# Kernel optimization log

Measured on AMD Instinct MI355X. Metric: run time of the kernel, lower is better.

Reference implementation:

```python
import jax, jax.numpy as jnp
import numpy as np

N, E = 20000, 640000
LATENT, HID, OUT, HEADS = 512, 256, 128, 2
NEG_SLOPE = 0.2


def setup_inputs() -> dict:
    key = jax.random.key(0)
    ks = jax.random.split(key, 12)
    s = 0.02
    return {
        "z": jax.random.normal(ks[0], (N, LATENT), dtype=jnp.float32),
        "edge_index": jax.random.randint(ks[1], (2, E), 0, N, dtype=jnp.int64),
        "W1": jax.random.normal(ks[2], (LATENT, HID), dtype=jnp.float32) * s,
        "b1": jnp.zeros((HID,), dtype=jnp.float32),
        "W2": jax.random.normal(ks[3], (HID, HID * HEADS), dtype=jnp.float32) * s,
        "b2": jnp.zeros((HID * HEADS,), dtype=jnp.float32),
        "Wg": jax.random.normal(ks[4], (HID * HEADS, HEADS * OUT), dtype=jnp.float32) * s,
        "att_src": jax.random.normal(ks[5], (HEADS, OUT), dtype=jnp.float32) * s,
        "att_dst": jax.random.normal(ks[6], (HEADS, OUT), dtype=jnp.float32) * s,
        "bias_g": jnp.zeros((HEADS * OUT,), dtype=jnp.float32),
        "W3": jax.random.normal(ks[7], (OUT * HEADS, 512), dtype=jnp.float32) * s,
        "b3": jnp.zeros((512,), dtype=jnp.float32),
    }


def _gat_conv(x, edge_index, Wg, att_src, att_dst, bias_g):
    n = x.shape[0]
    # add self loops (PyG GATConv default add_self_loops=True)
    loops = jnp.tile(jnp.arange(n, dtype=edge_index.dtype)[None, :], (2, 1))
    ei = jnp.concatenate([edge_index, loops], axis=1)
    src, dst = ei[0], ei[1]
    xp = (x @ Wg).reshape(n, HEADS, OUT)          # [N,H,C]
    a_src = jnp.einsum('nhc,hc->nh', xp, att_src)  # [N,H]
    a_dst = jnp.einsum('nhc,hc->nh', xp, att_dst)
    alpha = jax.nn.leaky_relu(a_src[src] + a_dst[dst], NEG_SLOPE)  # [E+N,H]
    amax = jax.ops.segment_max(alpha, dst, num_segments=n)
    alpha = jnp.exp(alpha - amax[dst])
    denom = jax.ops.segment_sum(alpha, dst, num_segments=n)
    alpha = alpha / jnp.maximum(denom[dst], 1e-16)
    msg = xp[src] * alpha[:, :, None]              # [E+N,H,C]
    out = jax.ops.segment_sum(msg, dst, num_segments=n)  # [N,H,C]
    return out.reshape(n, HEADS * OUT) + bias_g


def reference(z, edge_index, W1, b1, W2, b2, Wg, att_src, att_dst, bias_g, W3, b3):
    x = jax.nn.relu(z @ W1 + b1)
    x = jax.nn.relu(x @ W2 + b2)
    x = _gat_conv(x, edge_index, Wg, att_src, att_dst, bias_g)
    return x @ W3 + b3
```

## Files before the change

kernel.cpp:

```cpp
#include <hip/hip_runtime.h>
#include <hip/hip_bf16.h>
#include <float.h>

#define N_NODES 20000
#define LATENT  512
#define HID     256
#define OUT_C   128
#define HEADS   2
#define HC      256
#define NEG_SLOPE 0.2f

typedef _Float16 half8 __attribute__((ext_vector_type(8)));
typedef __attribute__((ext_vector_type(4))) float f32x4;

__device__ __forceinline__ ushort f2h(float v) {
    _Float16 h = (_Float16)v;
    return *(ushort*)&h;
}
__device__ __forceinline__ float h2f(ushort u) {
    _Float16 h = *(_Float16*)&u;
    return (float)h;
}

__device__ __forceinline__ void gl_lds16(const ushort* g, ushort* l) {
    __builtin_amdgcn_global_load_lds(
        (const __attribute__((address_space(1))) unsigned int*)g,
        (__attribute__((address_space(3))) unsigned int*)l, 16, 0, 0);
}

template<int BN>
__global__ __launch_bounds__(256) void gemm_f16(
    const ushort* __restrict__ A, const ushort* __restrict__ BT,
    const float* __restrict__ bias,
    float* __restrict__ Cf, ushort* __restrict__ Ch,
    int M, int N, int K, int relu)
{
    constexpr int NI  = BN / 32;
    constexpr int BUF = 4096 + BN * 32;
    __shared__ ushort lds[2 * BUF];
    ushort* buf0 = lds;
    ushort* buf1 = lds + BUF;

    const int t = threadIdx.x;
    const int l = t & 63;
    const int w = t >> 6;
    const int wm = (w >> 1) * 64;
    const int wn = (w & 1) * (BN / 2);
    const int lm = l & 15;
    const int q  = l >> 4;
    const int q4 = q * 4;

    const int row0 = blockIdx.x * 128;
    const int col0 = blockIdx.y * BN;

    const int jr0 = w * 16 + (l >> 2);
    const int gsh = (((l & 3) ^ ((l >> 4) & 3)) << 3);
    const ushort* gA0 = A + (size_t)(row0 + jr0) * K + gsh;
    const ushort* gA1 = gA0 + (size_t)64 * K;
    const ushort* gB0 = BT + (size_t)(col0 + jr0) * K + gsh;
    const ushort* gB1 = gB0 + (size_t)64 * K;
    const int dA0 = w * 512, dA1 = (4 + w) * 512;
    const int dB0 = 4096 + w * 512, dB1 = 4096 + (4 + w) * 512;

    const int csw = ((q ^ ((lm >> 2) & 3)) << 3);

    const f32x4 zf = {0.f, 0.f, 0.f, 0.f};
    f32x4 acc[4][NI];
    #pragma unroll
    for (int i = 0; i < 4; ++i)
        #pragma unroll
        for (int j = 0; j < NI; ++j) acc[i][j] = zf;

    auto issue = [&](int kk, ushort* B) {
        gl_lds16(gA0 + kk, B + dA0);
        gl_lds16(gA1 + kk, B + dA1);
        gl_lds16(gB0 + kk, B + dB0);
        if (BN == 128) gl_lds16(gB1 + kk, B + dB1);
    };

    auto compute = [&](const ushort* B) {
        half8 bf[NI];
        #pragma unroll
        for (int ni = 0; ni < NI; ++ni) {
            const int boff = (wn + ni * 16 + lm) * 32 + csw;
            bf[ni] = *(const half8*)&B[4096 + boff];
        }
        #pragma unroll
        for (int mi = 0; mi < 4; ++mi) {
            const int aoff = (wm + mi * 16 + lm) * 32 + csw;
            half8 af = *(const half8*)&B[aoff];
            #pragma unroll
            for (int ni = 0; ni < NI; ++ni)
                acc[mi][ni] = __builtin_amdgcn_mfma_f32_16x16x32_f16(
                    af, bf[ni], acc[mi][ni], 0, 0, 0);
        }
    };

    issue(0, buf0);
    __syncthreads();
    for (int k0 = 0; k0 < K; k0 += 64) {
        issue(k0 + 32, buf1);
        compute(buf0);
        __syncthreads();
        if (k0 + 64 < K) issue(k0 + 64, buf0);
        compute(buf1);
        __syncthreads();
    }

    #pragma unroll
    for (int mi = 0; mi < 4; ++mi) {
        #pragma unroll
        for (int ni = 0; ni < NI; ++ni) {
            const int col = col0 + wn + ni * 16 + lm;
            const float bv = bias ? bias[col] : 0.f;
            #pragma unroll
            for (int r = 0; r < 4; ++r) {
                const int row = row0 + wm + mi * 16 + q4 + r;
                if (row >= M) continue;
                float v = acc[mi][ni][r] + bv;
                if (relu) v = fmaxf(v, 0.f);
                const size_t idx = (size_t)row * N + col;
                if (Cf) Cf[idx] = v;
                if (Ch) Ch[idx] = f2h(v);
            }
        }
    }
}

__global__ __launch_bounds__(256) void cvt_zero_kernel(
    const float* __restrict__ x, ushort* __restrict__ o, int n4,
    int* deg, int* cursor, int n)
{
    int i = blockIdx.x * 256 + threadIdx.x;
    if (i < n) { deg[i] = 0; cursor[i] = 0; }
    if (i >= n4) return;
    float4 v = ((const float4*)x)[i];
    ((ushort4*)o)[i] = make_ushort4(f2h(v.x), f2h(v.y), f2h(v.z), f2h(v.w));
}

__global__ __launch_bounds__(256) void transpose_cvt4_kernel(
    const float* __restrict__ W1, const float* __restrict__ W2,
    const float* __restrict__ Wg, const float* __restrict__ W3,
    ushort* __restrict__ T1, ushort* __restrict__ T2,
    ushort* __restrict__ Tg, ushort* __restrict__ T3)
{
    int idx = blockIdx.x * 256 + threadIdx.x;
    int which = idx >> 17, i = idx & 131071;
    const float* W; ushort* T; int K, N;
    if (which == 0)      { W = W1; T = T1; K = 512; N = 256; }
    else if (which == 1) { W = W2; T = T2; K = 256; N = 512; }
    else if (which == 2) { W = Wg; T = Tg; K = 512; N = 256; }
    else                 { W = W3; T = T3; K = 256; N = 512; }
    int k = i / N, n = i - k * N;
    T[(size_t)n * K + k] = f2h(W[i]);
}

__global__ __launch_bounds__(256) void att_kernel(
    const ushort* __restrict__ xp, const float* __restrict__ att_src,
    const float* __restrict__ att_dst,
    float* __restrict__ a_src, float* __restrict__ a_dst, int n)
{
    int node = (blockIdx.x * 256 + threadIdx.x) >> 6;
    int lane = threadIdx.x & 63;
    if (node >= n) return;
    int h = lane >> 5, lh = lane & 31;
    int c = h * OUT_C + lh * 4;
    const ushort4 v = *(const ushort4*)(xp + (size_t)node * HC + c);
    const float4 as = *(const float4*)(att_src + c);
    const float4 ad = *(const float4*)(att_dst + c);
    float x0 = h2f(v.x), x1 = h2f(v.y), x2 = h2f(v.z), x3 = h2f(v.w);
    float s1 = x0 * as.x + x1 * as.y + x2 * as.z + x3 * as.w;
    float s2 = x0 * ad.x + x1 * ad.y + x2 * ad.z + x3 * ad.w;
    #pragma unroll
    for (int off = 16; off > 0; off >>= 1) {
        s1 += __shfl_xor(s1, off);
        s2 += __shfl_xor(s2, off);
    }
    if (lh == 0) { a_src[2 * node + h] = s1; a_dst[2 * node + h] = s2; }
}

__global__ __launch_bounds__(256) void hist_kernel(
    const int* __restrict__ dst, int* deg, int E_real, int ET)
{
    int e = blockIdx.x * blockDim.x + threadIdx.x;
    if (e >= ET) return;
    int d = (e < E_real) ? dst[e] : (e - E_real);
    atomicAdd(&deg[d], 1);
}

__global__ __launch_bounds__(256) void scan_kernel(
    const int* __restrict__ deg, int* __restrict__ rowptr, int n)
{
    __shared__ int part[256];
    const int t = threadIdx.x;
    const int chunk = (n + 255) / 256;
    const int lo = t * chunk;
    const int hi = min(lo + chunk, n);
    int s = 0;
    for (int i = lo; i < hi; ++i) s += deg[i];
    part[t] = s;
    __syncthreads();
    #pragma unroll
    for (int off = 1; off < 256; off <<= 1) {
        int add = (t >= off) ? part[t - off] : 0;
        __syncthreads();
        part[t] += add;
        __syncthreads();
    }
    int run = part[t] - s;
    for (int i = lo; i < hi; ++i) { rowptr[i] = run; run += deg[i]; }
    if (t == 255) rowptr[n] = part[255];
}

__global__ __launch_bounds__(256) void scatter_kernel(
    const int* __restrict__ src, const int* __restrict__ dst,
    const int* __restrict__ rowptr, int* cursor,
    int* __restrict__ sorted_src, int E_real, int ET)
{
    int e = blockIdx.x * blockDim.x + threadIdx.x;
    if (e >= ET) return;
    int s, d;
    if (e < E_real) { s = src[e]; d = dst[e]; }
    else            { s = e - E_real; d = s; }
    int pos = rowptr[d] + atomicAdd(&cursor[d], 1);
    sorted_src[pos] = s;
}

__global__ __launch_bounds__(64) void gat_aggregate(
    const int* __restrict__ rowptr, const int* __restrict__ sorted_src,
    const float* __restrict__ a_src, const float* __restrict__ a_dst,
    const ushort* __restrict__ xp, const float* __restrict__ bias_g,
    ushort* __restrict__ xg)
{
    __shared__ float s_w[2][64];
    __shared__ int   s_off[64];

    const int d = blockIdx.x;
    const int lane = threadIdx.x;
    const int h = lane >> 5;
    const int start = rowptr[d], end = rowptr[d + 1];

    const float ad0 = a_dst[2 * d + 0];
    const float ad1 = a_dst[2 * d + 1];

    float m0 = -FLT_MAX, m1 = -FLT_MAX;
    for (int e = start + lane; e < end; e += 64) {
        int s = sorted_src[e];
        float v0 = a_src[2 * s + 0] + ad0;
        float v1 = a_src[2 * s + 1] + ad1;
        v0 = (v0 > 0.f) ? v0 : NEG_SLOPE * v0;
        v1 = (v1 > 0.f) ? v1 : NEG_SLOPE * v1;
        m0 = fmaxf(m0, v0);
        m1 = fmaxf(m1, v1);
    }
    #pragma unroll
    for (int off = 32; off > 0; off >>= 1) {
        m0 = fmaxf(m0, __shfl_xor(m0, off));
        m1 = fmaxf(m1, __shfl_xor(m1, off));
    }

    float4 acc = make_float4(0.f, 0.f, 0.f, 0.f);
    float denom = 0.f;
    for (int e0 = start; e0 < end; e0 += 64) {
        int cnt = min(64, end - e0);
        if (lane < cnt) {
            int s = sorted_src[e0 + lane];
            float v0 = a_src[2 * s + 0] + ad0;
            float v1 = a_src[2 * s + 1] + ad1;
            v0 = (v0 > 0.f) ? v0 : NEG_SLOPE * v0;
            v1 = (v1 > 0.f) ? v1 : NEG_SLOPE * v1;
            s_w[0][lane] = expf(v0 - m0);
            s_w[1][lane] = expf(v1 - m1);
            s_off[lane] = s * HC;
        }
        __syncthreads();
        for (int j = 0; j < cnt; ++j) {
            float w = s_w[h][j];
            const ushort4 v = *(const ushort4*)(xp + s_off[j] + 4 * lane);
            denom += w;
            acc.x += w * h2f(v.x); acc.y += w * h2f(v.y);
            acc.z += w * h2f(v.z); acc.w += w * h2f(v.w);
        }
        __syncthreads();
    }

    float inv = 1.f / fmaxf(denom, 1e-16f);
    int c = 4 * lane;
    float4 bg = *(const float4*)(bias_g + c);
    const size_t base = ((size_t)d * HC + c) >> 2;
    ((ushort4*)xg)[base] = make_ushort4(
        f2h(acc.x * inv + bg.x), f2h(acc.y * inv + bg.y),
        f2h(acc.z * inv + bg.z), f2h(acc.w * inv + bg.w));
}

extern "C" void kernel_launch(void* const* d_in, const int* in_sizes, int n_in,
                              void* d_out, int out_size, void* d_ws, size_t ws_size,
                              hipStream_t stream)
{
    const float* z       = (const float*)d_in[0];
    const int*   ei      = (const int*)d_in[1];
    const float* W1      = (const float*)d_in[2];
    const float* b1      = (const float*)d_in[3];
    const float* W2      = (const float*)d_in[4];
    const float* b2      = (const float*)d_in[5];
    const float* Wg      = (const float*)d_in[6];
    const float* att_src = (const float*)d_in[7];
    const float* att_dst = (const float*)d_in[8];
    const float* bias_g  = (const float*)d_in[9];
    const float* W3      = (const float*)d_in[10];
    const float* b3      = (const float*)d_in[11];
    float* out = (float*)d_out;

    const int n = N_NODES;
    const int E_real = in_sizes[1] / 2;
    const int ET = E_real + n;
    const int* src = ei;
    const int* dst = ei + E_real;

    char* p = (char*)d_ws;
    auto alloc = [&](size_t bytes) {
        char* r = p;
        p += (bytes + 63) & ~(size_t)63;
        return r;
    };
    const int np = n + 128;
    ushort* z_f16  = (ushort*)alloc((size_t)np * LATENT * 2);
    ushort* x1_f16 = (ushort*)alloc((size_t)np * HID * 2);
    ushort* xp_f16 = (ushort*)alloc((size_t)n * HC * 2);
    ushort* W1T = (ushort*)alloc((size_t)LATENT * HID * 2);
    ushort* W2T = (ushort*)alloc((size_t)HID * 512 * 2);
    ushort* WgT = (ushort*)alloc((size_t)512 * HC * 2);
    ushort* W3T = (ushort*)alloc((size_t)HC * 512 * 2);
    float* a_src = (float*)alloc((size_t)2 * n * 4);
    float* a_dst = (float*)alloc((size_t)2 * n * 4);
    int* deg        = (int*)alloc((size_t)n * 4);
    int* rowptr     = (int*)alloc(((size_t)n + 1) * 4);
    int* cursor     = (int*)alloc((size_t)n * 4);
    int* sorted_src = (int*)alloc((size_t)ET * 4);
    ushort* x2_f16 = z_f16;
    ushort* xg_f16 = x1_f16;

    const int gm128 = (n + 127) / 128;

    cvt_zero_kernel<<<(n * LATENT / 4 + 255) / 256, 256, 0, stream>>>(
        z, z_f16, n * LATENT / 4, deg, cursor, n);
    transpose_cvt4_kernel<<<(4 * 131072) / 256, 256, 0, stream>>>(
        W1, W2, Wg, W3, W1T, W2T, WgT, W3T);

    gemm_f16<64><<<dim3(gm128, HID / 64), 256, 0, stream>>>(
        z_f16, W1T, b1, nullptr, x1_f16, n, HID, LATENT, 1);
    gemm_f16<64><<<dim3(gm128, 512 / 64), 256, 0, stream>>>(
        x1_f16, W2T, b2, nullptr, x2_f16, n, 512, HID, 1);
    gemm_f16<64><<<dim3(gm128, HC / 64), 256, 0, stream>>>(
        x2_f16, WgT, nullptr, nullptr, xp_f16, n, HC, 512, 0);

    att_kernel<<<(n * 64 + 255) / 256, 256, 0, stream>>>(
        xp_f16, att_src, att_dst, a_src, a_dst, n);
    hist_kernel<<<(ET + 255) / 256, 256, 0, stream>>>(dst, deg, E_real, ET);
    scan_kernel<<<1, 256, 0, stream>>>(deg, rowptr, n);
    scatter_kernel<<<(ET + 255) / 256, 256, 0, stream>>>(
        src, dst, rowptr, cursor, sorted_src, E_real, ET);
    gat_aggregate<<<n, 64, 0, stream>>>(
        rowptr, sorted_src, a_src, a_dst, xp_f16, bias_g, xg_f16);

    gemm_f16<64><<<dim3(gm128, 512 / 64), 256, 0, stream>>>(
        xg_f16, W3T, b3, out, nullptr, n, 512, HC, 0);
}
```

Before: 338.5 us.

## Parametrize GEMM K-tile, fuse histogram into weight transpose, unroll GAT gather

The GEMM kernel gains a BK template parameter, with generalized swizzled LDS loads and inner k-halves. K=256 GEMMs use BK=64 to halve the barrier count, while others keep BK=32. The edge histogram is folded into the weight transpose/convert kernel as extra blocks, and the CSR build is moved ahead of the GEMMs, removing one launch. The GAT aggregation loop is unrolled by four to put more independent gathers in flight. The larger LDS footprint for BK=64 may reduce occupancy.

```diff
diff --git a/kernel.cpp b/kernel.cpp
--- a/kernel.cpp
+++ b/kernel.cpp
@@ -28,7 +28,7 @@
         (__attribute__((address_space(3))) unsigned int*)l, 16, 0, 0);
 }
 
-template<int BN>
+template<int BN, int BK>
 __global__ __launch_bounds__(256) void gemm_f16(
     const ushort* __restrict__ A, const ushort* __restrict__ BT,
     const float* __restrict__ bias,
@@ -36,7 +36,13 @@
     int M, int N, int K, int relu)
 {
     constexpr int NI  = BN / 32;
-    constexpr int BUF = 4096 + BN * 32;
+    constexpr int CR  = BK / 8;
+    constexpr int RPI = 64 / CR;
+    constexpr int NAI = CR / 2;
+    constexpr int NBI = BN * CR / 256;
+    constexpr int KH  = BK / 32;
+    constexpr int BBASE = 128 * BK;
+    constexpr int BUF = (128 + BN) * BK;
     __shared__ ushort lds[2 * BUF];
     ushort* buf0 = lds;
     ushort* buf1 = lds + BUF;
@@ -53,16 +59,24 @@
     const int row0 = blockIdx.x * 128;
     const int col0 = blockIdx.y * BN;
 
-    const int jr0 = w * 16 + (l >> 2);
-    const int gsh = (((l & 3) ^ ((l >> 4) & 3)) << 3);
-    const ushort* gA0 = A + (size_t)(row0 + jr0) * K + gsh;
-    const ushort* gA1 = gA0 + (size_t)64 * K;
-    const ushort* gB0 = BT + (size_t)(col0 + jr0) * K + gsh;
-    const ushort* gB1 = gB0 + (size_t)64 * K;
-    const int dA0 = w * 512, dA1 = (4 + w) * 512;
-    const int dB0 = 4096 + w * 512, dB1 = 4096 + (4 + w) * 512;
-
-    const int csw = ((q ^ ((lm >> 2) & 3)) << 3);
+    const int rli = l / CR;
+    const int gch = ((l % CR) ^ (rli & (CR - 1)));
+    const ushort* gA[NAI];
+    int dA[NAI];
+    #pragma unroll
+    for (int j = 0; j < NAI; ++j) {
+        const int i = j * 4 + w;
+        gA[j] = A + (size_t)(row0 + i * RPI + rli) * K + gch * 8;
+        dA[j] = i * 512;
+    }
+    const ushort* gB[NBI];
+    int dB[NBI];
+    #pragma unroll
+    for (int j = 0; j < NBI; ++j) {
+        const int i = j * 4 + w;
+        gB[j] = BT + (size_t)(col0 + i * RPI + rli) * K + gch * 8;
+        dB[j] = BBASE + i * 512;
+    }
 
     const f32x4 zf = {0.f, 0.f, 0.f, 0.f};
     f32x4 acc[4][NI];
@@ -72,37 +86,38 @@
         for (int j = 0; j < NI; ++j) acc[i][j] = zf;
 
     auto issue = [&](int kk, ushort* B) {
-        gl_lds16(gA0 + kk, B + dA0);
-        gl_lds16(gA1 + kk, B + dA1);
-        gl_lds16(gB0 + kk, B + dB0);
-        if (BN == 128) gl_lds16(gB1 + kk, B + dB1);
+        #pragma unroll
+        for (int j = 0; j < NAI; ++j) gl_lds16(gA[j] + kk, B + dA[j]);
+        #pragma unroll
+        for (int j = 0; j < NBI; ++j) gl_lds16(gB[j] + kk, B + dB[j]);
     };
 
     auto compute = [&](const ushort* B) {
-        half8 bf[NI];
-        #pragma unroll
-        for (int ni = 0; ni < NI; ++ni) {
-            const int boff = (wn + ni * 16 + lm) * 32 + csw;
-            bf[ni] = *(const half8*)&B[4096 + boff];
-        }
-        #pragma unroll
-        for (int mi = 0; mi < 4; ++mi) {
-            const int aoff = (wm + mi * 16 + lm) * 32 + csw;
-            half8 af = *(const half8*)&B[aoff];
+        #pragma unroll
+        for (int kh = 0; kh < KH; ++kh) {
+            const int csw = (((kh * 4 + q) ^ (lm & (CR - 1))) << 3);
+            half8 bf[NI];
             #pragma unroll
             for (int ni = 0; ni < NI; ++ni)
-                acc[mi][ni] = __builtin_amdgcn_mfma_f32_16x16x32_f16(
-                    af, bf[ni], acc[mi][ni], 0, 0, 0);
+                bf[ni] = *(const half8*)&B[BBASE + (wn + ni * 16 + lm) * BK + csw];
+            #pragma unroll
+            for (int mi = 0; mi < 4; ++mi) {
+                half8 af = *(const half8*)&B[(wm + mi * 16 + lm) * BK + csw];
+                #pragma unroll
+                for (int ni = 0; ni < NI; ++ni)
+                    acc[mi][ni] = __builtin_amdgcn_mfma_f32_16x16x32_f16(
+                        af, bf[ni], acc[mi][ni], 0, 0, 0);
+            }
         }
     };
 
     issue(0, buf0);
     __syncthreads();
-    for (int k0 = 0; k0 < K; k0 += 64) {
-        issue(k0 + 32, buf1);
+    for (int k0 = 0; k0 < K; k0 += 2 * BK) {
+        issue(k0 + BK, buf1);
         compute(buf0);
         __syncthreads();
-        if (k0 + 64 < K) issue(k0 + 64, buf0);
+        if (k0 + 2 * BK < K) issue(k0 + 2 * BK, buf0);
         compute(buf1);
         __syncthreads();
     }
@@ -138,12 +153,20 @@
     ((ushort4*)o)[i] = make_ushort4(f2h(v.x), f2h(v.y), f2h(v.z), f2h(v.w));
 }
 
-__global__ __launch_bounds__(256) void transpose_cvt4_kernel(
+__global__ __launch_bounds__(256) void transpose_cvt4_hist_kernel(
     const float* __restrict__ W1, const float* __restrict__ W2,
     const float* __restrict__ Wg, const float* __restrict__ W3,
     ushort* __restrict__ T1, ushort* __restrict__ T2,
-    ushort* __restrict__ Tg, ushort* __restrict__ T3)
-{
+    ushort* __restrict__ Tg, ushort* __restrict__ T3,
+    const int* __restrict__ dst, int* deg, int E_real, int ET)
+{
+    if (blockIdx.x >= 2048) {
+        int e = (blockIdx.x - 2048) * 256 + threadIdx.x;
+        if (e >= ET) return;
+        int d = (e < E_real) ? dst[e] : (e - E_real);
+        atomicAdd(&deg[d], 1);
+        return;
+    }
     int idx = blockIdx.x * 256 + threadIdx.x;
     int which = idx >> 17, i = idx & 131071;
     const float* W; ushort* T; int K, N;
@@ -179,15 +202,6 @@
     if (lh == 0) { a_src[2 * node + h] = s1; a_dst[2 * node + h] = s2; }
 }
 
-__global__ __launch_bounds__(256) void hist_kernel(
-    const int* __restrict__ dst, int* deg, int E_real, int ET)
-{
-    int e = blockIdx.x * blockDim.x + threadIdx.x;
-    if (e >= ET) return;
-    int d = (e < E_real) ? dst[e] : (e - E_real);
-    atomicAdd(&deg[d], 1);
-}
-
 __global__ __launch_bounds__(256) void scan_kernel(
     const int* __restrict__ deg, int* __restrict__ rowptr, int n)
 {
@@ -261,6 +275,7 @@
 
     float4 acc = make_float4(0.f, 0.f, 0.f, 0.f);
     float denom = 0.f;
+    const int cl = 4 * lane;
     for (int e0 = start; e0 < end; e0 += 64) {
         int cnt = min(64, end - e0);
         if (lane < cnt) {
@@ -274,9 +289,23 @@
             s_off[lane] = s * HC;
         }
         __syncthreads();
-        for (int j = 0; j < cnt; ++j) {
-            float w = s_w[h][j];
-            const ushort4 v = *(const ushort4*)(xp + s_off[j] + 4 * lane);
+        int j = 0;
+        for (; j + 4 <= cnt; j += 4) {
+            const ushort4 v0 = *(const ushort4*)(xp + s_off[j + 0] + cl);
+            const ushort4 v1 = *(const ushort4*)(xp + s_off[j + 1] + cl);
+            const ushort4 v2 = *(const ushort4*)(xp + s_off[j + 2] + cl);
+            const ushort4 v3 = *(const ushort4*)(xp + s_off[j + 3] + cl);
+            const float w0 = s_w[h][j + 0], w1 = s_w[h][j + 1];
+            const float w2 = s_w[h][j + 2], w3 = s_w[h][j + 3];
+            denom += (w0 + w1) + (w2 + w3);
+            acc.x += w0 * h2f(v0.x) + w1 * h2f(v1.x) + w2 * h2f(v2.x) + w3 * h2f(v3.x);
+            acc.y += w0 * h2f(v0.y) + w1 * h2f(v1.y) + w2 * h2f(v2.y) + w3 * h2f(v3.y);
+            acc.z += w0 * h2f(v0.z) + w1 * h2f(v1.z) + w2 * h2f(v2.z) + w3 * h2f(v3.z);
+            acc.w += w0 * h2f(v0.w) + w1 * h2f(v1.w) + w2 * h2f(v2.w) + w3 * h2f(v3.w);
+        }
+        for (; j < cnt; ++j) {
+            const float w = s_w[h][j];
+            const ushort4 v = *(const ushort4*)(xp + s_off[j] + cl);
             denom += w;
             acc.x += w * h2f(v.x); acc.y += w * h2f(v.y);
             acc.z += w * h2f(v.z); acc.w += w * h2f(v.w);
@@ -285,9 +314,8 @@
     }
 
     float inv = 1.f / fmaxf(denom, 1e-16f);
-    int c = 4 * lane;
-    float4 bg = *(const float4*)(bias_g + c);
-    const size_t base = ((size_t)d * HC + c) >> 2;
+    float4 bg = *(const float4*)(bias_g + cl);
+    const size_t base = ((size_t)d * HC + cl) >> 2;
     ((ushort4*)xg)[base] = make_ushort4(
         f2h(acc.x * inv + bg.x), f2h(acc.y * inv + bg.y),
         f2h(acc.z * inv + bg.z), f2h(acc.w * inv + bg.w));
@@ -341,28 +369,28 @@
     ushort* xg_f16 = x1_f16;
 
     const int gm128 = (n + 127) / 128;
+    const int histb = (ET + 255) / 256;
 
     cvt_zero_kernel<<<(n * LATENT / 4 + 255) / 256, 256, 0, stream>>>(
         z, z_f16, n * LATENT / 4, deg, cursor, n);
-    transpose_cvt4_kernel<<<(4 * 131072) / 256, 256, 0, stream>>>(
-        W1, W2, Wg, W3, W1T, W2T, WgT, W3T);
-
-    gemm_f16<64><<<dim3(gm128, HID / 64), 256, 0, stream>>>(
+    transpose_cvt4_hist_kernel<<<2048 + histb, 256, 0, stream>>>(
+        W1, W2, Wg, W3, W1T, W2T, WgT, W3T, dst, deg, E_real, ET);
+    scan_kernel<<<1, 256, 0, stream>>>(deg, rowptr, n);
+    scatter_kernel<<<histb, 256, 0, stream>>>(
+        src, dst, rowptr, cursor, sorted_src, E_real, ET);
+
+    gemm_f16<64, 32><<<dim3(gm128, HID / 64), 256, 0, stream>>>(
         z_f16, W1T, b1, nullptr, x1_f16, n, HID, LATENT, 1);
-    gemm_f16<64><<<dim3(gm128, 512 / 64), 256, 0, stream>>>(
+    gemm_f16<64, 64><<<dim3(gm128, 512 / 64), 256, 0, stream>>>(
         x1_f16, W2T, b2, nullptr, x2_f16, n, 512, HID, 1);
-    gemm_f16<64><<<dim3(gm128, HC / 64), 256, 0, stream>>>(
+    gemm_f16<64, 32><<<dim3(gm128, HC / 64), 256, 0, stream>>>(
         x2_f16, WgT, nullptr, nullptr, xp_f16, n, HC, 512, 0);
 
     att_kernel<<<(n * 64 + 255) / 256, 256, 0, stream>>>(
         xp_f16, att_src, att_dst, a_src, a_dst, n);
-    hist_kernel<<<(ET + 255) / 256, 256, 0, stream>>>(dst, deg, E_real, ET);
-    scan_kernel<<<1, 256, 0, stream>>>(deg, rowptr, n);
-    scatter_kernel<<<(ET + 255) / 256, 256, 0, stream>>>(
-        src, dst, rowptr, cursor, sorted_src, E_real, ET);
     gat_aggregate<<<n, 64, 0, stream>>>(
         rowptr, sorted_src, a_src, a_dst, xp_f16, bias_g, xg_f16);
 
-    gemm_f16<64><<<dim3(gm128, 512 / 64), 256, 0, stream>>>(
+    gemm_f16<64, 64><<<dim3(gm128, 512 / 64), 256, 0, stream>>>(
         xg_f16, W3T, b3, out, nullptr, n, 512, HC, 0);
 }
```

Result: no change. 343.9 us (+1.6%).
